# Performance work log

Hardware: AMD Instinct MI355X
Metric: run time of the kernel (lower is better)

The kernel has to match this reference:

```python
import jax, jax.numpy as jnp
import numpy as np

N = 50000   # nodes
E = 800000  # edges
IND = 128   # in_dim
HID = 128   # num_hidden
NH = 4      # heads
HD = HID // NH
L = 2       # num_layers
SLOPE = 0.2


def setup_inputs() -> dict:
    key = jax.random.key(0)
    ks = jax.random.split(key, 32)
    rn = lambda k, shp, s=1.0: jax.random.normal(k, shp, jnp.float32) * s
    W = 0.08  # weight scale (xavier-ish)
    return {
        "x_t": rn(ks[0], (N, IND)),
        "time_embed": rn(ks[1], (N, HID)),
        "src": jax.random.randint(ks[2], (E,), 0, N),
        "dst": jax.random.randint(ks[3], (E,), 0, N),
        "W_init": rn(ks[4], (IND + HID, HID), W), "b_init": jnp.zeros((HID,), jnp.float32),
        "Wsrc_down": rn(ks[5], (L, HID, HID), W), "bsrc_down": jnp.zeros((L, HID), jnp.float32),
        "Wdst_down": rn(ks[6], (L, HID, HID), W), "bdst_down": jnp.zeros((L, HID), jnp.float32),
        "attn_down": rn(ks[7], (L, NH, HD), W), "bout_down": jnp.zeros((L, HID), jnp.float32),
        "Wsrc_mid": rn(ks[8], (HID, HID), W), "bsrc_mid": jnp.zeros((HID,), jnp.float32),
        "Wdst_mid": rn(ks[9], (HID, HID), W), "bdst_mid": jnp.zeros((HID,), jnp.float32),
        "attn_mid": rn(ks[10], (NH, HD), W), "bout_mid": jnp.zeros((HID,), jnp.float32),
        "Wsrc_up": rn(ks[11], (L, 2 * HID, HID), W), "bsrc_up": jnp.zeros((L, HID), jnp.float32),
        "Wdst_up": rn(ks[12], (L, 2 * HID, HID), W), "bdst_up": jnp.zeros((L, HID), jnp.float32),
        "attn_up": rn(ks[13], (L, NH, HD), W), "bout_up": jnp.zeros((L, HID), jnp.float32),
        "W_fin": rn(ks[14], (HID, HID), W), "b_fin": jnp.zeros((HID,), jnp.float32),
    }


def gatv2_layer(h, Wsrc, bsrc, Wdst, bdst, attn, bout, src, dst):
    # GATv2Conv (DGL semantics, eval mode / no dropout), flatten(1) included.
    fs = (h @ Wsrc + bsrc).reshape(-1, NH, HD)  # [N,H,D]
    fd = (h @ Wdst + bdst).reshape(-1, NH, HD)
    e = jax.nn.leaky_relu(fs[src] + fd[dst], SLOPE)           # [E,H,D]
    logits = jnp.einsum('ehd,hd->eh', e, attn)                # [E,H]
    m = jax.ops.segment_max(logits, dst, num_segments=N)      # [N,H]
    m = jnp.where(jnp.isfinite(m), m, 0.0)                    # zero-in-degree safety
    p = jnp.exp(logits - m[dst])                              # [E,H]
    s = jax.ops.segment_sum(p, dst, num_segments=N)           # [N,H]
    alpha = p / (s[dst] + 1e-9)                               # edge softmax per dst
    out = jax.ops.segment_sum(alpha[:, :, None] * fs[src], dst, num_segments=N)
    out = out.reshape(-1, HID) + bout
    return jax.nn.gelu(out)


def reference(x_t, time_embed, src, dst,
              W_init, b_init,
              Wsrc_down, bsrc_down, Wdst_down, bdst_down, attn_down, bout_down,
              Wsrc_mid, bsrc_mid, Wdst_mid, bdst_mid, attn_mid, bout_mid,
              Wsrc_up, bsrc_up, Wdst_up, bdst_up, attn_up, bout_up,
              W_fin, b_fin):
    h = jnp.concatenate([x_t, time_embed], axis=1)
    h = jax.nn.gelu(h @ W_init + b_init)
    skips = []
    for i in range(L):
        skips.append(h)
        h = gatv2_layer(h, Wsrc_down[i], bsrc_down[i], Wdst_down[i], bdst_down[i],
                        attn_down[i], bout_down[i], src, dst)
    h = gatv2_layer(h, Wsrc_mid, bsrc_mid, Wdst_mid, bdst_mid, attn_mid, bout_mid, src, dst)
    for i in range(L):
        h = jnp.concatenate([h, skips[L - 1 - i]], axis=1)
        h = gatv2_layer(h, Wsrc_up[i], bsrc_up[i], Wdst_up[i], bdst_up[i],
                        attn_up[i], bout_up[i], src, dst)
    out = h @ W_fin + b_fin
    return (out, h)
```

## Files before the change

### kernel.cpp

```cpp
#include <hip/hip_runtime.h>
#include <hip/hip_bf16.h>
#include <math.h>

#define HIDDIM 128
#define MT 64

typedef float f32x4 __attribute__((ext_vector_type(4)));
typedef int i32x4 __attribute__((ext_vector_type(4)));
typedef short bf16x8 __attribute__((ext_vector_type(8)));

__device__ inline float gelu_f(float x) {
  float x3 = x * x * x;
  return 0.5f * x * (1.0f + tanhf(0.7978845608028654f * (x + 0.044715f * x3)));
}

__device__ inline void split_bf16(float a, unsigned short& hi, unsigned short& lo) {
  unsigned u = __float_as_uint(a);
  unsigned r = (u + 0x7FFFu + ((u >> 16) & 1u)) & 0xFFFF0000u;
  hi = (unsigned short)(r >> 16);
  float rem = a - __uint_as_float(r);
  unsigned u2 = __float_as_uint(rem);
  lo = (unsigned short)((u2 + 0x7FFFu + ((u2 >> 16) & 1u)) >> 16);
}

__device__ inline void split_pair(float a0, float a1, unsigned& hp, unsigned& lp) {
  unsigned u0 = __float_as_uint(a0), u1 = __float_as_uint(a1);
  unsigned r0 = (u0 + 0x7FFFu + ((u0 >> 16) & 1u)) & 0xFFFF0000u;
  unsigned r1 = (u1 + 0x7FFFu + ((u1 >> 16) & 1u)) & 0xFFFF0000u;
  hp = (r0 >> 16) | r1;
  float m0 = a0 - __uint_as_float(r0);
  float m1 = a1 - __uint_as_float(r1);
  unsigned v0 = __float_as_uint(m0), v1 = __float_as_uint(m1);
  unsigned s0 = v0 + 0x7FFFu + ((v0 >> 16) & 1u);
  unsigned s1 = (v1 + 0x7FFFu + ((v1 >> 16) & 1u)) & 0xFFFF0000u;
  lp = (s0 >> 16) | s1;
}

__global__ void detect_dtype(const unsigned short* __restrict__ raw, int* __restrict__ flag) {
  __shared__ int cnt;
  if (threadIdx.x == 0) cnt = 0;
  __syncthreads();
  int c = 0;
  for (int i = threadIdx.x; i < 8192; i += 256) {
    int ex = (raw[i] >> 7) & 0xFF;
    if (ex >= 0xC0) c++;
  }
  atomicAdd(&cnt, c);
  __syncthreads();
  if (threadIdx.x == 0) flag[0] = (cnt > 64) ? 1 : 0;
}

__global__ void cvt_to_f32_2(const void* __restrict__ in0, const void* __restrict__ in1,
                             float* __restrict__ out0, float* __restrict__ out1,
                             int n, const int* __restrict__ flag) {
  int i = blockIdx.x * 256 + threadIdx.x;
  if (i < n) {
    out0[i] = flag[0] ? ((const float*)in0)[i]
                      : __bfloat162float(((const __hip_bfloat16*)in0)[i]);
  } else if (i < 2 * n) {
    int j = i - n;
    out1[j] = flag[0] ? ((const float*)in1)[j]
                      : __bfloat162float(((const __hip_bfloat16*)in1)[j]);
  }
}

#define NITEMS 14
struct StageArgs {
  const void* src[NITEMS];
  int off[NITEMS];
  int n[NITEMS];
  int blk0[NITEMS];
};
__global__ void stage_params(StageArgs a, float* __restrict__ params,
                             const int* __restrict__ flag) {
  int b = blockIdx.x;
  int it = 0;
  while (it + 1 < NITEMS && a.blk0[it + 1] <= b) ++it;
  int i = (b - a.blk0[it]) * 256 + threadIdx.x;
  if (i < a.n[it]) {
    params[a.off[it] + i] = flag[0]
        ? ((const float*)a.src[it])[i]
        : __bfloat162float(((const __hip_bfloat16*)a.src[it])[i]);
  }
}

#define NSPLIT 12
struct SplitArgs {
  const void* src[NSPLIT];
  int eoff[NSPLIT];
  int soff[NSPLIT];
  int K[NSPLIT];
  int blk0[NSPLIT];
};
__global__ void split_weights(SplitArgs a,
                              unsigned short* __restrict__ whi,
                              unsigned short* __restrict__ wlo,
                              const int* __restrict__ flag) {
  int b = blockIdx.x, it = 0;
  while (it + 1 < NSPLIT && a.blk0[it + 1] <= b) ++it;
  int i = (b - a.blk0[it]) * 256 + threadIdx.x;
  int K = a.K[it];
  if (i < K * 128) {
    float v = flag[0]
        ? ((const float*)a.src[it])[a.eoff[it] + i]
        : __bfloat162float(((const __hip_bfloat16*)a.src[it])[a.eoff[it] + i]);
    int k = i >> 7, col = i & 127;
    unsigned short h, lo;
    split_bf16(v, h, lo);
    int o = a.soff[it] + col * K + k;
    whi[o] = h;
    wlo[o] = lo;
  }
}

template <int KT, int FUSED, int ACT>
__global__ __launch_bounds__(256, 3) void gemm_mfma(
    const float* __restrict__ A1, const float* __restrict__ A2,
    const unsigned short* __restrict__ Whi0, const unsigned short* __restrict__ Wlo0,
    const unsigned short* __restrict__ Whi1, const unsigned short* __restrict__ Wlo1,
    const float* __restrict__ b0, const float* __restrict__ b1,
    float* __restrict__ C0, float* __restrict__ C1, int M) {
  constexpr int K = KT * 32;
  constexpr int CT = FUSED ? 8 : 4;
  const int t = threadIdx.x;
  const int w = t >> 6, l = t & 63;
  const int m0 = blockIdx.x * 64;
  const int rbase = (w & 1) * 32;
  const int chalf = w >> 1;
  const unsigned short* whi = (FUSED && chalf) ? Whi1 : Whi0;
  const unsigned short* wlo = (FUSED && chalf) ? Wlo1 : Wlo0;
  const int cbase = FUSED ? 0 : chalf * 64;
  float* Cw = (FUSED && chalf) ? C1 : C0;
  const float* bw = (FUSED && chalf) ? b1 : b0;
  const int lr = l & 15;
  const int lk = l >> 4;

  int arow[2];
#pragma unroll
  for (int rt = 0; rt < 2; ++rt) arow[rt] = min(m0 + rbase + rt * 16 + lr, M - 1);

  f32x4 acc[2][CT];
#pragma unroll
  for (int rt = 0; rt < 2; ++rt)
#pragma unroll
    for (int ct = 0; ct < CT; ++ct) acc[rt][ct] = (f32x4){0.f, 0.f, 0.f, 0.f};

#pragma unroll
  for (int s = 0; s < KT; ++s) {
    const float* Ab = (KT == 8 && s >= 4) ? A2 : A1;
    const int krel = (KT == 8 ? (s & 3) : s) * 32 + lk * 8;

    bf16x8 ah[2], al[2];
#pragma unroll
    for (int rt = 0; rt < 2; ++rt) {
      const float* ap = &Ab[(size_t)arow[rt] * 128 + krel];
      float4 v0 = *(const float4*)ap;
      float4 v1 = *(const float4*)(ap + 4);
      i32x4 hv, lv;
      unsigned hp, lp;
      split_pair(v0.x, v0.y, hp, lp); hv[0] = (int)hp; lv[0] = (int)lp;
      split_pair(v0.z, v0.w, hp, lp); hv[1] = (int)hp; lv[1] = (int)lp;
      split_pair(v1.x, v1.y, hp, lp); hv[2] = (int)hp; lv[2] = (int)lp;
      split_pair(v1.z, v1.w, hp, lp); hv[3] = (int)hp; lv[3] = (int)lp;
      ah[rt] = __builtin_bit_cast(bf16x8, hv);
      al[rt] = __builtin_bit_cast(bf16x8, lv);
    }

    bf16x8 bh[CT], bl[CT];
#pragma unroll
    for (int ct = 0; ct < CT; ++ct) {
      size_t off = (size_t)(cbase + ct * 16 + lr) * K + s * 32 + lk * 8;
      bh[ct] = *(const bf16x8*)&whi[off];
      bl[ct] = *(const bf16x8*)&wlo[off];
    }

#pragma unroll
    for (int rt = 0; rt < 2; ++rt)
#pragma unroll
      for (int ct = 0; ct < CT; ++ct) {
        acc[rt][ct] = __builtin_amdgcn_mfma_f32_16x16x32_bf16(ah[rt], bh[ct], acc[rt][ct], 0, 0, 0);
        acc[rt][ct] = __builtin_amdgcn_mfma_f32_16x16x32_bf16(ah[rt], bl[ct], acc[rt][ct], 0, 0, 0);
        acc[rt][ct] = __builtin_amdgcn_mfma_f32_16x16x32_bf16(al[rt], bh[ct], acc[rt][ct], 0, 0, 0);
      }
  }

#pragma unroll
  for (int ct = 0; ct < CT; ++ct) {
    int col = cbase + ct * 16 + lr;
    float bias = bw[col];
#pragma unroll
    for (int rt = 0; rt < 2; ++rt) {
      int rowb = m0 + rbase + rt * 16 + lk * 4;
#pragma unroll
      for (int r = 0; r < 4; ++r) {
        int row = rowb + r;
        if (row < M) {
          float v = acc[rt][ct][r] + bias;
          if (ACT) v = gelu_f(v);
          Cw[(size_t)row * 128 + col] = v;
        }
      }
    }
  }
}

__global__ void count_deg(const int* __restrict__ dst, int* __restrict__ deg, int E) {
  int e = blockIdx.x * 256 + threadIdx.x;
  if (e < E) atomicAdd(&deg[dst[e]], 1);
}

__global__ __launch_bounds__(1024) void scan_blocks(
    const int* __restrict__ deg, int* __restrict__ rowptr,
    int* __restrict__ cursor, int* __restrict__ bsum, int N) {
  __shared__ int buf[1024];
  int i = blockIdx.x * 1024 + threadIdx.x;
  int v = (i < N) ? deg[i] : 0;
  buf[threadIdx.x] = v;
  __syncthreads();
  for (int off = 1; off < 1024; off <<= 1) {
    int add = (threadIdx.x >= (unsigned)off) ? buf[threadIdx.x - off] : 0;
    __syncthreads();
    buf[threadIdx.x] += add;
    __syncthreads();
  }
  int excl = buf[threadIdx.x] - v;
  if (i < N) { rowptr[i] = excl; cursor[i] = excl; }
  if (threadIdx.x == 1023) bsum[blockIdx.x] = buf[1023];
}

__global__ __launch_bounds__(1024) void scan_partials(int* __restrict__ bsum, int nb) {
  __shared__ int buf[1024];
  int v = (threadIdx.x < (unsigned)nb) ? bsum[threadIdx.x] : 0;
  buf[threadIdx.x] = v;
  __syncthreads();
  for (int off = 1; off < 1024; off <<= 1) {
    int add = (threadIdx.x >= (unsigned)off) ? buf[threadIdx.x - off] : 0;
    __syncthreads();
    buf[threadIdx.x] += add;
    __syncthreads();
  }
  int excl = buf[threadIdx.x] - v;
  if (threadIdx.x < (unsigned)nb) bsum[threadIdx.x] = excl;
  if (threadIdx.x == 1023) bsum[nb] = buf[1023];
}

__global__ void add_offsets(int* __restrict__ rowptr, int* __restrict__ cursor,
                            const int* __restrict__ bsum, int N, int nb) {
  int i = blockIdx.x * 256 + threadIdx.x;
  if (i < N) {
    int add = bsum[i >> 10];
    rowptr[i] += add;
    cursor[i] += add;
  }
  if (i == 0) rowptr[N] = bsum[nb];
}

__global__ void place_edges(const int* __restrict__ src, const int* __restrict__ dst,
                            int* __restrict__ cursor, int* __restrict__ colsrc, int E) {
  int e = blockIdx.x * 256 + threadIdx.x;
  if (e < E) {
    int pos = atomicAdd(&cursor[dst[e]], 1);
    colsrc[pos] = src[e];
  }
}

__global__ __launch_bounds__(256) void gat_agg(
    const float* __restrict__ fs, const float* __restrict__ fd,
    const int* __restrict__ rowptr, const int* __restrict__ colsrc,
    const float* __restrict__ attn, const float* __restrict__ bout,
    float* __restrict__ hout, int N, int E) {
  int wv = threadIdx.x >> 6, lane = threadIdx.x & 63;
  int n = blockIdx.x * 4 + wv;
  if (n >= N) return;
  int half = lane >> 5;
  int fb = (lane & 31) * 4;
  float4 fdv = *(const float4*)&fd[(size_t)n * HIDDIM + fb];
  float a0 = attn[fb], a1 = attn[fb + 1], a2 = attn[fb + 2], a3 = attn[fb + 3];
  int e0 = rowptr[n], e1 = rowptr[n + 1];
  e0 = max(0, min(e0, E));
  e1 = max(e0, min(e1, E));
  float s = 0.f, ax = 0.f, ay = 0.f, az = 0.f, aw = 0.f;
  for (int c0 = e0; c0 < e1; c0 += 64) {
    int cn = min(64, e1 - c0);
    int myidx = (lane < cn) ? colsrc[c0 + lane] : 0;
    myidx = ((unsigned)myidx < (unsigned)N) ? myidx : 0;
    int iters = (cn + 3) >> 2;
    for (int it = 0; it < iters; ++it) {
      int jA = 4 * it + half;
      int jB = jA + 2;
      int sA = __shfl(myidx, min(jA, cn - 1));
      int sB = __shfl(myidx, min(jB, cn - 1));
      float4 fA = *(const float4*)&fs[(size_t)sA * HIDDIM + fb];
      float4 fB = *(const float4*)&fs[(size_t)sB * HIDDIM + fb];
      float v0, v1, v2, v3, lA, lB;
      v0 = fA.x + fdv.x; v0 = v0 > 0.f ? v0 : 0.2f * v0;
      v1 = fA.y + fdv.y; v1 = v1 > 0.f ? v1 : 0.2f * v1;
      v2 = fA.z + fdv.z; v2 = v2 > 0.f ? v2 : 0.2f * v2;
      v3 = fA.w + fdv.w; v3 = v3 > 0.f ? v3 : 0.2f * v3;
      lA = fmaf(v0, a0, fmaf(v1, a1, fmaf(v2, a2, v3 * a3)));
      v0 = fB.x + fdv.x; v0 = v0 > 0.f ? v0 : 0.2f * v0;
      v1 = fB.y + fdv.y; v1 = v1 > 0.f ? v1 : 0.2f * v1;
      v2 = fB.z + fdv.z; v2 = v2 > 0.f ? v2 : 0.2f * v2;
      v3 = fB.w + fdv.w; v3 = v3 > 0.f ? v3 : 0.2f * v3;
      lB = fmaf(v0, a0, fmaf(v1, a1, fmaf(v2, a2, v3 * a3)));
      lA += __shfl_xor(lA, 1); lA += __shfl_xor(lA, 2); lA += __shfl_xor(lA, 4);
      lB += __shfl_xor(lB, 1); lB += __shfl_xor(lB, 2); lB += __shfl_xor(lB, 4);
      lA = fminf(lA, 60.f);
      lB = fminf(lB, 60.f);
      float pA = (jA < cn) ? __expf(lA) : 0.f;
      float pB = (jB < cn) ? __expf(lB) : 0.f;
      s += pA + pB;
      ax = fmaf(pA, fA.x, fmaf(pB, fB.x, ax));
      ay = fmaf(pA, fA.y, fmaf(pB, fB.y, ay));
      az = fmaf(pA, fA.z, fmaf(pB, fB.z, az));
      aw = fmaf(pA, fA.w, fmaf(pB, fB.w, aw));
    }
  }
  s += __shfl_xor(s, 32);
  ax += __shfl_xor(ax, 32); ay += __shfl_xor(ay, 32);
  az += __shfl_xor(az, 32); aw += __shfl_xor(aw, 32);
  if (half == 0) {
    float inv = 1.f / (s + 1e-9f);
    float o0 = gelu_f(fmaf(ax, inv, bout[fb]));
    float o1 = gelu_f(fmaf(ay, inv, bout[fb + 1]));
    float o2 = gelu_f(fmaf(az, inv, bout[fb + 2]));
    float o3 = gelu_f(fmaf(aw, inv, bout[fb + 3]));
    *(float4*)&hout[(size_t)n * HIDDIM + fb] = make_float4(o0, o1, o2, o3);
  }
}

__global__ void store_out(const float* __restrict__ og, const float* __restrict__ h,
                          void* __restrict__ dout, int n, const int* __restrict__ flag) {
  int i = blockIdx.x * 256 + threadIdx.x;
  if (i >= n) return;
  if (flag[0]) {
    ((float*)dout)[i] = og[i];
    ((float*)dout)[n + i] = h[i];
  } else {
    ((__hip_bfloat16*)dout)[i] = __float2bfloat16(og[i]);
    ((__hip_bfloat16*)dout)[n + i] = __float2bfloat16(h[i]);
  }
}

#define PB_INIT    0
#define PBSRC_DOWN 128
#define PBDST_DOWN 384
#define PATTN_DOWN 640
#define PBOUT_DOWN 896
#define PBSRC_MID  1152
#define PBDST_MID  1280
#define PATTN_MID  1408
#define PBOUT_MID  1536
#define PBSRC_UP   1664
#define PBDST_UP   1920
#define PATTN_UP   2176
#define PBOUT_UP   2432
#define PB_FIN     2688
#define PARAMS_TOTAL 2816

#define SP_W_INIT    0
#define SP_WSRC_D0   32768
#define SP_WSRC_D1   49152
#define SP_WDST_D0   65536
#define SP_WDST_D1   81920
#define SP_WSRC_MID  98304
#define SP_WDST_MID  114688
#define SP_WSRC_U0   131072
#define SP_WSRC_U1   163840
#define SP_WDST_U0   196608
#define SP_WDST_U1   229376
#define SP_W_FIN     262144
#define SPLIT_TOTAL  278528

extern "C" void kernel_launch(void* const* d_in, const int* in_sizes, int n_in,
                              void* d_out, int out_size, void* d_ws, size_t ws_size,
                              hipStream_t stream) {
  const int N = in_sizes[1] / HIDDIM;
  const int E = in_sizes[2];
  const int* src = (const int*)d_in[2];
  const int* dst = (const int*)d_in[3];

  char* p = (char*)d_ws;
  auto carve = [&](size_t bytes) {
    void* r = (void*)p;
    p += (bytes + 255) & ~(size_t)255;
    return r;
  };
  int* flag     = (int*)carve(256);
  float* params = (float*)carve((size_t)PARAMS_TOTAL * 4);
  unsigned short* whi = (unsigned short*)carve((size_t)SPLIT_TOTAL * 2);
  unsigned short* wlo = (unsigned short*)carve((size_t)SPLIT_TOTAL * 2);
  int* deg      = (int*)carve((size_t)N * 4);
  int* rowptr   = (int*)carve((size_t)(N + 1) * 4);
  int* cursor   = (int*)carve((size_t)N * 4);
  int* bsum     = (int*)carve(1032 * 4);
  int* colsrc   = (int*)carve((size_t)E * 4);
  float* hA     = (float*)carve((size_t)N * HIDDIM * 4);
  float* hB     = (float*)carve((size_t)N * HIDDIM * 4);
  float* hC     = (float*)carve((size_t)N * HIDDIM * 4);
  float* fs     = (float*)carve((size_t)N * HIDDIM * 4);
  float* fd     = (float*)carve((size_t)N * HIDDIM * 4);

  detect_dtype<<<1, 256, 0, stream>>>((const unsigned short*)d_in[0], flag);

  static const int idx[NITEMS] = {5, 7, 9, 10, 11, 13, 15, 16, 17, 19, 21, 22, 23, 25};
  static const int off[NITEMS] = {
    PB_INIT, PBSRC_DOWN, PBDST_DOWN, PATTN_DOWN, PBOUT_DOWN,
    PBSRC_MID, PBDST_MID, PATTN_MID, PBOUT_MID,
    PBSRC_UP, PBDST_UP, PATTN_UP, PBOUT_UP, PB_FIN};
  static const int cnt[NITEMS] = {
    128, 256, 256, 256, 256, 128, 128, 128, 128, 256, 256, 256, 256, 128};
  StageArgs sa;
  int nb = 0;
  for (int i = 0; i < NITEMS; ++i) {
    sa.src[i] = d_in[idx[i]];
    sa.off[i] = off[i];
    sa.n[i] = cnt[i];
    sa.blk0[i] = nb;
    nb += (cnt[i] + 255) / 256;
  }
  stage_params<<<nb, 256, 0, stream>>>(sa, params, flag);

  static const int widx[NSPLIT]  = {4, 6, 6, 8, 8, 12, 14, 18, 18, 20, 20, 24};
  static const int weoff[NSPLIT] = {0, 0, 16384, 0, 16384, 0, 0, 0, 32768, 0, 32768, 0};
  static const int wsoff[NSPLIT] = {
    SP_W_INIT, SP_WSRC_D0, SP_WSRC_D1, SP_WDST_D0, SP_WDST_D1,
    SP_WSRC_MID, SP_WDST_MID, SP_WSRC_U0, SP_WSRC_U1, SP_WDST_U0, SP_WDST_U1,
    SP_W_FIN};
  static const int wK[NSPLIT] = {256, 128, 128, 128, 128, 128, 128, 256, 256, 256, 256, 128};
  SplitArgs spa;
  int snb = 0;
  for (int i = 0; i < NSPLIT; ++i) {
    spa.src[i] = d_in[widx[i]];
    spa.eoff[i] = weoff[i];
    spa.soff[i] = wsoff[i];
    spa.K[i] = wK[i];
    spa.blk0[i] = snb;
    snb += (wK[i] * 128 + 255) / 256;
  }
  split_weights<<<snb, 256, 0, stream>>>(spa, whi, wlo, flag);

  float* xc = fs;
  float* tc = fd;
  cvt_to_f32_2<<<(2 * N * HIDDIM + 255) / 256, 256, 0, stream>>>(
      d_in[0], d_in[1], xc, tc, N * HIDDIM, flag);

  hipMemsetAsync(deg, 0, (size_t)N * 4, stream);
  count_deg<<<(E + 255) / 256, 256, 0, stream>>>(dst, deg, E);
  int nsb = (N + 1023) / 1024;
  scan_blocks<<<nsb, 1024, 0, stream>>>(deg, rowptr, cursor, bsum, N);
  scan_partials<<<1, 1024, 0, stream>>>(bsum, nsb);
  add_offsets<<<(N + 255) / 256, 256, 0, stream>>>(rowptr, cursor, bsum, N, nsb);
  place_edges<<<(E + 255) / 256, 256, 0, stream>>>(src, dst, cursor, colsrc, E);

  dim3 gb((N + MT - 1) / MT);
  dim3 ga((N + 3) / 4);
  const float* P = params;

  gemm_mfma<8, 0, 1><<<gb, 256, 0, stream>>>(
      xc, tc, whi + SP_W_INIT, wlo + SP_W_INIT, nullptr, nullptr,
      P + PB_INIT, nullptr, hA, nullptr, N);

  auto gat_layer = [&](const float* ha, const float* hb, int spsrc, int spdst,
                       const float* bsrc, const float* bdst,
                       const float* attn, const float* bout, float* hout) {
    if (hb)
      gemm_mfma<8, 1, 0><<<gb, 256, 0, stream>>>(
          ha, hb, whi + spsrc, wlo + spsrc, whi + spdst, wlo + spdst,
          bsrc, bdst, fs, fd, N);
    else
      gemm_mfma<4, 1, 0><<<gb, 256, 0, stream>>>(
          ha, nullptr, whi + spsrc, wlo + spsrc, whi + spdst, wlo + spdst,
          bsrc, bdst, fs, fd, N);
    gat_agg<<<ga, 256, 0, stream>>>(fs, fd, rowptr, colsrc, attn, bout, hout, N, E);
  };

  gat_layer(hA, nullptr, SP_WSRC_D0, SP_WDST_D0, P + PBSRC_DOWN, P + PBDST_DOWN,
            P + PATTN_DOWN, P + PBOUT_DOWN, hB);
  gat_layer(hB, nullptr, SP_WSRC_D1, SP_WDST_D1, P + PBSRC_DOWN + 128,
            P + PBDST_DOWN + 128, P + PATTN_DOWN + 128, P + PBOUT_DOWN + 128, hC);
  gat_layer(hC, nullptr, SP_WSRC_MID, SP_WDST_MID, P + PBSRC_MID, P + PBDST_MID,
            P + PATTN_MID, P + PBOUT_MID, hC);
  gat_layer(hC, hB, SP_WSRC_U0, SP_WDST_U0, P + PBSRC_UP, P + PBDST_UP,
            P + PATTN_UP, P + PBOUT_UP, hC);
  gat_layer(hC, hA, SP_WSRC_U1, SP_WDST_U1, P + PBSRC_UP + 128, P + PBDST_UP + 128,
            P + PATTN_UP + 128, P + PBOUT_UP + 128, hC);

  float* outg = hB;
  gemm_mfma<4, 0, 0><<<gb, 256, 0, stream>>>(
      hC, nullptr, whi + SP_W_FIN, wlo + SP_W_FIN, nullptr, nullptr,
      P + PB_FIN, nullptr, outg, nullptr, N);
  store_out<<<(N * HIDDIM + 255) / 256, 256, 0, stream>>>(outg, hC, d_out, N * HIDDIM, flag);
}
```

Baseline: 1.023 ms.

## Keep GEMM weights register-resident with persistent grid-stride row tiles

Replaces the per-block GEMM, which reloaded weight fragments from global memory every K-step, with a persistent kernel. Each wave loads its weight slice into registers once and loops over 32-row tiles with a grid-stride loop. K=256 GEMMs are split into two K=128 launches, the second accumulating into the output with bias and activation applied at the end. The goal is to cut weight reload traffic and raise MFMA density, at the cost of higher register pressure (launch bounds lowered to 2), extra launches, and an extra read-modify-write of the output for the split GEMMs.

```diff
diff --git a/kernel.cpp b/kernel.cpp
--- a/kernel.cpp
+++ b/kernel.cpp
@@ -3,7 +3,6 @@
 #include <math.h>
 
 #define HIDDIM 128
-#define MT 64
 
 typedef float f32x4 __attribute__((ext_vector_type(4)));
 typedef int i32x4 __attribute__((ext_vector_type(4)));
@@ -113,91 +112,108 @@
   }
 }
 
-template <int KT, int FUSED, int ACT>
-__global__ __launch_bounds__(256, 3) void gemm_mfma(
-    const float* __restrict__ A1, const float* __restrict__ A2,
+template <int FUSED, int FINAL, int ACT, int ACCUM, int KS>
+__global__ __launch_bounds__(256, 2) void gemm_ws(
+    const float* __restrict__ A,
     const unsigned short* __restrict__ Whi0, const unsigned short* __restrict__ Wlo0,
     const unsigned short* __restrict__ Whi1, const unsigned short* __restrict__ Wlo1,
     const float* __restrict__ b0, const float* __restrict__ b1,
     float* __restrict__ C0, float* __restrict__ C1, int M) {
-  constexpr int K = KT * 32;
-  constexpr int CT = FUSED ? 8 : 4;
+  constexpr int CT = FUSED ? 4 : 2;
   const int t = threadIdx.x;
   const int w = t >> 6, l = t & 63;
-  const int m0 = blockIdx.x * 64;
-  const int rbase = (w & 1) * 32;
-  const int chalf = w >> 1;
-  const unsigned short* whi = (FUSED && chalf) ? Whi1 : Whi0;
-  const unsigned short* wlo = (FUSED && chalf) ? Wlo1 : Wlo0;
-  const int cbase = FUSED ? 0 : chalf * 64;
-  float* Cw = (FUSED && chalf) ? C1 : C0;
-  const float* bw = (FUSED && chalf) ? b1 : b0;
-  const int lr = l & 15;
-  const int lk = l >> 4;
-
-  int arow[2];
-#pragma unroll
-  for (int rt = 0; rt < 2; ++rt) arow[rt] = min(m0 + rbase + rt * 16 + lr, M - 1);
-
-  f32x4 acc[2][CT];
-#pragma unroll
-  for (int rt = 0; rt < 2; ++rt)
-#pragma unroll
-    for (int ct = 0; ct < CT; ++ct) acc[rt][ct] = (f32x4){0.f, 0.f, 0.f, 0.f};
-
-#pragma unroll
-  for (int s = 0; s < KT; ++s) {
-    const float* Ab = (KT == 8 && s >= 4) ? A2 : A1;
-    const int krel = (KT == 8 ? (s & 3) : s) * 32 + lk * 8;
-
-    bf16x8 ah[2], al[2];
+  const int lr = l & 15, lk = l >> 4;
+  const unsigned short* whi = Whi0;
+  const unsigned short* wlo = Wlo0;
+  const float* bw = b0;
+  float* Cw = C0;
+  int cbase;
+  if (FUSED) {
+    if (w >> 1) { whi = Whi1; wlo = Wlo1; bw = b1; Cw = C1; }
+    cbase = (w & 1) * 64;
+  } else {
+    cbase = w * 32;
+  }
+
+  bf16x8 wh[CT][4], wl[CT][4];
+#pragma unroll
+  for (int ct = 0; ct < CT; ++ct)
+#pragma unroll
+    for (int s = 0; s < 4; ++s) {
+      size_t off = (size_t)(cbase + ct * 16 + lr) * KS + s * 32 + lk * 8;
+      wh[ct][s] = *(const bf16x8*)&whi[off];
+      wl[ct][s] = *(const bf16x8*)&wlo[off];
+    }
+
+  f32x4 bias[CT];
+  if (FINAL) {
+#pragma unroll
+    for (int ct = 0; ct < CT; ++ct)
+      bias[ct] = *(const f32x4*)&bw[cbase + ct * 16 + lk * 4];
+  }
+
+  const int ntiles = (M + 31) >> 5;
+  for (int tb = blockIdx.x; tb < ntiles; tb += gridDim.x) {
+    int row[2];
+#pragma unroll
+    for (int rt = 0; rt < 2; ++rt) row[rt] = min(tb * 32 + rt * 16 + lr, M - 1);
+
+    float4 raw[2][4][2];
+#pragma unroll
+    for (int rt = 0; rt < 2; ++rt)
+#pragma unroll
+      for (int s = 0; s < 4; ++s) {
+        const float* ap = &A[(size_t)row[rt] * 128 + s * 32 + lk * 8];
+        raw[rt][s][0] = *(const float4*)ap;
+        raw[rt][s][1] = *(const float4*)(ap + 4);
+      }
+
+    f32x4 acc[2][CT];
+#pragma unroll
+    for (int rt = 0; rt < 2; ++rt)
+#pragma unroll
+      for (int ct = 0; ct < CT; ++ct) acc[rt][ct] = (f32x4){0.f, 0.f, 0.f, 0.f};
+
+#pragma unroll
+    for (int s = 0; s < 4; ++s) {
+      bf16x8 ah[2], al[2];
+#pragma unroll
+      for (int rt = 0; rt < 2; ++rt) {
+        float4 v0 = raw[rt][s][0], v1 = raw[rt][s][1];
+        i32x4 hv, lv;
+        unsigned hp, lp;
+        split_pair(v0.x, v0.y, hp, lp); hv[0] = (int)hp; lv[0] = (int)lp;
+        split_pair(v0.z, v0.w, hp, lp); hv[1] = (int)hp; lv[1] = (int)lp;
+        split_pair(v1.x, v1.y, hp, lp); hv[2] = (int)hp; lv[2] = (int)lp;
+        split_pair(v1.z, v1.w, hp, lp); hv[3] = (int)hp; lv[3] = (int)lp;
+        ah[rt] = __builtin_bit_cast(bf16x8, hv);
+        al[rt] = __builtin_bit_cast(bf16x8, lv);
+      }
+#pragma unroll
+      for (int rt = 0; rt < 2; ++rt)
+#pragma unroll
+        for (int ct = 0; ct < CT; ++ct) {
+          acc[rt][ct] = __builtin_amdgcn_mfma_f32_16x16x32_bf16(wh[ct][s], ah[rt], acc[rt][ct], 0, 0, 0);
+          acc[rt][ct] = __builtin_amdgcn_mfma_f32_16x16x32_bf16(wh[ct][s], al[rt], acc[rt][ct], 0, 0, 0);
+          acc[rt][ct] = __builtin_amdgcn_mfma_f32_16x16x32_bf16(wl[ct][s], ah[rt], acc[rt][ct], 0, 0, 0);
+        }
+    }
+
 #pragma unroll
     for (int rt = 0; rt < 2; ++rt) {
-      const float* ap = &Ab[(size_t)arow[rt] * 128 + krel];
-      float4 v0 = *(const float4*)ap;
-      float4 v1 = *(const float4*)(ap + 4);
-      i32x4 hv, lv;
-      unsigned hp, lp;
-      split_pair(v0.x, v0.y, hp, lp); hv[0] = (int)hp; lv[0] = (int)lp;
-      split_pair(v0.z, v0.w, hp, lp); hv[1] = (int)hp; lv[1] = (int)lp;
-      split_pair(v1.x, v1.y, hp, lp); hv[2] = (int)hp; lv[2] = (int)lp;
-      split_pair(v1.z, v1.w, hp, lp); hv[3] = (int)hp; lv[3] = (int)lp;
-      ah[rt] = __builtin_bit_cast(bf16x8, hv);
-      al[rt] = __builtin_bit_cast(bf16x8, lv);
-    }
-
-    bf16x8 bh[CT], bl[CT];
-#pragma unroll
-    for (int ct = 0; ct < CT; ++ct) {
-      size_t off = (size_t)(cbase + ct * 16 + lr) * K + s * 32 + lk * 8;
-      bh[ct] = *(const bf16x8*)&whi[off];
-      bl[ct] = *(const bf16x8*)&wlo[off];
-    }
-
-#pragma unroll
-    for (int rt = 0; rt < 2; ++rt)
-#pragma unroll
-      for (int ct = 0; ct < CT; ++ct) {
-        acc[rt][ct] = __builtin_amdgcn_mfma_f32_16x16x32_bf16(ah[rt], bh[ct], acc[rt][ct], 0, 0, 0);
-        acc[rt][ct] = __builtin_amdgcn_mfma_f32_16x16x32_bf16(ah[rt], bl[ct], acc[rt][ct], 0, 0, 0);
-        acc[rt][ct] = __builtin_amdgcn_mfma_f32_16x16x32_bf16(al[rt], bh[ct], acc[rt][ct], 0, 0, 0);
-      }
-  }
-
-#pragma unroll
-  for (int ct = 0; ct < CT; ++ct) {
-    int col = cbase + ct * 16 + lr;
-    float bias = bw[col];
-#pragma unroll
-    for (int rt = 0; rt < 2; ++rt) {
-      int rowb = m0 + rbase + rt * 16 + lk * 4;
-#pragma unroll
-      for (int r = 0; r < 4; ++r) {
-        int row = rowb + r;
-        if (row < M) {
-          float v = acc[rt][ct][r] + bias;
-          if (ACT) v = gelu_f(v);
-          Cw[(size_t)row * 128 + col] = v;
+      int r = tb * 32 + rt * 16 + lr;
+      if (r < M) {
+        float* cp = &Cw[(size_t)r * 128 + cbase + lk * 4];
+#pragma unroll
+        for (int ct = 0; ct < CT; ++ct) {
+          f32x4 v = acc[rt][ct];
+          if (ACCUM) v += *(const f32x4*)(cp + ct * 16);
+          if (FINAL) v += bias[ct];
+          if (ACT) {
+            v[0] = gelu_f(v[0]); v[1] = gelu_f(v[1]);
+            v[2] = gelu_f(v[2]); v[3] = gelu_f(v[3]);
+          }
+          *(f32x4*)(cp + ct * 16) = v;
         }
       }
     }
@@ -453,42 +469,56 @@
   add_offsets<<<(N + 255) / 256, 256, 0, stream>>>(rowptr, cursor, bsum, N, nsb);
   place_edges<<<(E + 255) / 256, 256, 0, stream>>>(src, dst, cursor, colsrc, E);
 
-  dim3 gb((N + MT - 1) / MT);
+  const int ntiles = (N + 31) >> 5;
+  dim3 gw((unsigned)min(512, ntiles));
   dim3 ga((N + 3) / 4);
   const float* P = params;
-
-  gemm_mfma<8, 0, 1><<<gb, 256, 0, stream>>>(
-      xc, tc, whi + SP_W_INIT, wlo + SP_W_INIT, nullptr, nullptr,
+  const unsigned short* nh = nullptr;
+
+  gemm_ws<0, 0, 0, 0, 256><<<gw, 256, 0, stream>>>(
+      xc, whi + SP_W_INIT, wlo + SP_W_INIT, nh, nh,
+      nullptr, nullptr, hA, nullptr, N);
+  gemm_ws<0, 1, 1, 1, 256><<<gw, 256, 0, stream>>>(
+      tc, whi + SP_W_INIT + 128, wlo + SP_W_INIT + 128, nh, nh,
       P + PB_INIT, nullptr, hA, nullptr, N);
 
-  auto gat_layer = [&](const float* ha, const float* hb, int spsrc, int spdst,
-                       const float* bsrc, const float* bdst,
-                       const float* attn, const float* bout, float* hout) {
-    if (hb)
-      gemm_mfma<8, 1, 0><<<gb, 256, 0, stream>>>(
-          ha, hb, whi + spsrc, wlo + spsrc, whi + spdst, wlo + spdst,
-          bsrc, bdst, fs, fd, N);
-    else
-      gemm_mfma<4, 1, 0><<<gb, 256, 0, stream>>>(
-          ha, nullptr, whi + spsrc, wlo + spsrc, whi + spdst, wlo + spdst,
-          bsrc, bdst, fs, fd, N);
-    gat_agg<<<ga, 256, 0, stream>>>(fs, fd, rowptr, colsrc, attn, bout, hout, N, E);
-  };
-
-  gat_layer(hA, nullptr, SP_WSRC_D0, SP_WDST_D0, P + PBSRC_DOWN, P + PBDST_DOWN,
-            P + PATTN_DOWN, P + PBOUT_DOWN, hB);
-  gat_layer(hB, nullptr, SP_WSRC_D1, SP_WDST_D1, P + PBSRC_DOWN + 128,
-            P + PBDST_DOWN + 128, P + PATTN_DOWN + 128, P + PBOUT_DOWN + 128, hC);
-  gat_layer(hC, nullptr, SP_WSRC_MID, SP_WDST_MID, P + PBSRC_MID, P + PBDST_MID,
-            P + PATTN_MID, P + PBOUT_MID, hC);
-  gat_layer(hC, hB, SP_WSRC_U0, SP_WDST_U0, P + PBSRC_UP, P + PBDST_UP,
-            P + PATTN_UP, P + PBOUT_UP, hC);
-  gat_layer(hC, hA, SP_WSRC_U1, SP_WDST_U1, P + PBSRC_UP + 128, P + PBDST_UP + 128,
-            P + PATTN_UP + 128, P + PBOUT_UP + 128, hC);
+  gemm_ws<1, 1, 0, 0, 128><<<gw, 256, 0, stream>>>(
+      hA, whi + SP_WSRC_D0, wlo + SP_WSRC_D0, whi + SP_WDST_D0, wlo + SP_WDST_D0,
+      P + PBSRC_DOWN, P + PBDST_DOWN, fs, fd, N);
+  gat_agg<<<ga, 256, 0, stream>>>(fs, fd, rowptr, colsrc,
+                                  P + PATTN_DOWN, P + PBOUT_DOWN, hB, N, E);
+  gemm_ws<1, 1, 0, 0, 128><<<gw, 256, 0, stream>>>(
+      hB, whi + SP_WSRC_D1, wlo + SP_WSRC_D1, whi + SP_WDST_D1, wlo + SP_WDST_D1,
+      P + PBSRC_DOWN + 128, P + PBDST_DOWN + 128, fs, fd, N);
+  gat_agg<<<ga, 256, 0, stream>>>(fs, fd, rowptr, colsrc,
+                                  P + PATTN_DOWN + 128, P + PBOUT_DOWN + 128, hC, N, E);
+  gemm_ws<1, 1, 0, 0, 128><<<gw, 256, 0, stream>>>(
+      hC, whi + SP_WSRC_MID, wlo + SP_WSRC_MID, whi + SP_WDST_MID, wlo + SP_WDST_MID,
+      P + PBSRC_MID, P + PBDST_MID, fs, fd, N);
+  gat_agg<<<ga, 256, 0, stream>>>(fs, fd, rowptr, colsrc,
+                                  P + PATTN_MID, P + PBOUT_MID, hC, N, E);
+  gemm_ws<1, 0, 0, 0, 256><<<gw, 256, 0, stream>>>(
+      hC, whi + SP_WSRC_U0, wlo + SP_WSRC_U0, whi + SP_WDST_U0, wlo + SP_WDST_U0,
+      nullptr, nullptr, fs, fd, N);
+  gemm_ws<1, 1, 0, 1, 256><<<gw, 256, 0, stream>>>(
+      hB, whi + SP_WSRC_U0 + 128, wlo + SP_WSRC_U0 + 128,
+      whi + SP_WDST_U0 + 128, wlo + SP_WDST_U0 + 128,
+      P + PBSRC_UP, P + PBDST_UP, fs, fd, N);
+  gat_agg<<<ga, 256, 0, stream>>>(fs, fd, rowptr, colsrc,
+                                  P + PATTN_UP, P + PBOUT_UP, hC, N, E);
+  gemm_ws<1, 0, 0, 0, 256><<<gw, 256, 0, stream>>>(
+      hC, whi + SP_WSRC_U1, wlo + SP_WSRC_U1, whi + SP_WDST_U1, wlo + SP_WDST_U1,
+      nullptr, nullptr, fs, fd, N);
+  gemm_ws<1, 1, 0, 1, 256><<<gw, 256, 0, stream>>>(
+      hA, whi + SP_WSRC_U1 + 128, wlo + SP_WSRC_U1 + 128,
+      whi + SP_WDST_U1 + 128, wlo + SP_WDST_U1 + 128,
+      P + PBSRC_UP + 128, P + PBDST_UP + 128, fs, fd, N);
+  gat_agg<<<ga, 256, 0, stream>>>(fs, fd, rowptr, colsrc,
+                                  P + PATTN_UP + 128, P + PBOUT_UP + 128, hC, N, E);
 
   float* outg = hB;
-  gemm_mfma<4, 0, 0><<<gb, 256, 0, stream>>>(
-      hC, nullptr, whi + SP_W_FIN, wlo + SP_W_FIN, nullptr, nullptr,
+  gemm_ws<0, 1, 0, 0, 128><<<gw, 256, 0, stream>>>(
+      hC, whi + SP_W_FIN, wlo + SP_W_FIN, nh, nh,
       P + PB_FIN, nullptr, outg, nullptr, N);
   store_out<<<(N * HIDDIM + 255) / 256, 256, 0, stream>>>(outg, hC, d_out, N * HIDDIM, flag);
 }
```

After: 921.4 us. 1.11x faster.
